# Optimization experiments

Measured on AMD Instinct MI355X. Metric: run time of the kernel, lower is better.

The kernel has to match this reference:

```python
import jax, jax.numpy as jnp
import numpy as np

BETA = 0.25
EPS_NORM = 1e-12   # matches torch F.normalize eps
EPS_COS = 1e-6     # clamp floor for cos weight


def _l2_normalize(v, axis=-1):
    n = jnp.linalg.norm(v, axis=axis, keepdims=True)
    return v / jnp.maximum(n, EPS_NORM)


def setup_inputs() -> dict:
    key = jax.random.key(0)
    kx, kc = jax.random.split(key)
    x = jax.random.normal(kx, (64, 1024, 256), dtype=jnp.float32)
    codebook = jax.random.normal(kc, (4096, 256), dtype=jnp.float32)
    return {"x": x, "codebook": codebook}


def reference(x, codebook):
    # Normalize codebook rows (F.normalize(codebook, dim=-1)).
    cb_n = _l2_normalize(codebook)                     # [K, D]
    # Cosine distance: 1 - cos_sim(x, cb). Only sim matters for argmin.
    x_n = _l2_normalize(x)                             # [B, S, D]
    sim = jnp.einsum('bsd,kd->bsk', x_n, cb_n)         # [B, S, K]
    dists = 1.0 - sim
    ids = jnp.argmin(dists, axis=-1)                   # [B, S] int
    c_k = cb_n[ids]                                    # [B, S, D] gather
    # Cosine weight uses RAW x (x_norm = x in the torch code).
    cos_k = jnp.sum(x * c_k, axis=-1, keepdims=True)   # [B, S, 1]
    cos_k = jnp.maximum(cos_k, EPS_COS)
    weighted_emb = cos_k * c_k                         # [B, S, D]
    # Cosine quantization loss: codebook term + beta * commitment term,
    # each 1 - cos_sim with stop-gradient on the opposite operand.
    def cos_sim(a, b):
        return jnp.sum(_l2_normalize(a) * _l2_normalize(b), axis=-1)
    codebook_term = jnp.mean(1.0 - cos_sim(jax.lax.stop_gradient(x), c_k))
    commit_term = jnp.mean(1.0 - cos_sim(x, jax.lax.stop_gradient(c_k)))
    loss = codebook_term + BETA * commit_term
    return ids, weighted_emb, loss
```

## Files before the change

kernel.cpp:

```cpp
#include <hip/hip_runtime.h>
#include <math.h>
#include <stdint.h>


#define TOKENS 65536
#define DIM 256
#define KCB 4096

#define TB 256
#define DELTA_SCALE 0.03125f
#define LIST_CAP (1u << 21)
#define SCAP 4096
#define RBLOCKS 2048

typedef short bf16x8 __attribute__((ext_vector_type(8)));
typedef float f32x4 __attribute__((ext_vector_type(4)));

__device__ inline short f2bf(float f) {
    uint32_t u = __float_as_uint(f);
    u += 0x7FFF + ((u >> 16) & 1);
    return (short)(u >> 16);
}

__global__ void prep_all(const float* __restrict__ cb, const float* __restrict__ x,
                         float* __restrict__ cbn, short* __restrict__ cbh2,
                         float* __restrict__ xnorm, float* __restrict__ invnx) {
    int bid  = blockIdx.x;
    int w    = threadIdx.x >> 6;
    int lane = threadIdx.x & 63;
    if (bid < KCB / 4) {
        int row = bid * 4 + w;
        float4 v = *(const float4*)(cb + (size_t)row * DIM + lane * 4);
        float ss = v.x * v.x + v.y * v.y + v.z * v.z + v.w * v.w;
#pragma unroll
        for (int off = 32; off; off >>= 1) ss += __shfl_xor(ss, off);
        float scale = 1.0f / fmaxf(sqrtf(ss), 1e-12f);
        float4 o = {v.x * scale, v.y * scale, v.z * scale, v.w * scale};
        *(float4*)(cbn + (size_t)row * DIM + lane * 4) = o;
        short4 h = {f2bf(o.x), f2bf(o.y), f2bf(o.z), f2bf(o.w)};
        int g = row >> 4, l15 = row & 15;
        int kst = lane >> 3, q = (lane >> 1) & 3, jhalf = lane & 1;
        size_t dst = ((size_t)((g * 8 + kst) * 64 + q * 16 + l15)) * 8 + jhalf * 4;
        *(short4*)(cbh2 + dst) = h;
    } else {
        int row = (bid - KCB / 4) * 4 + w;
        float4 v = *(const float4*)(x + (size_t)row * DIM + lane * 4);
        float ss = v.x * v.x + v.y * v.y + v.z * v.z + v.w * v.w;
#pragma unroll
        for (int off = 32; off; off >>= 1) ss += __shfl_xor(ss, off);
        if (lane == 0) {
            float n = fmaxf(sqrtf(ss), 1e-12f);
            xnorm[row] = n;
            invnx[row] = 1.0f / n;
        }
    }
}

#define LOADB(buf, cti)                                                            \
    {                                                                              \
        const short* bp_ = cbh2 + (size_t)(ch * 128 + (cti)) * 4096 + lane * 8;    \
        _Pragma("unroll")                                                          \
        for (int j = 0; j < 8; ++j) buf[j] = *(const bf16x8*)(bp_ + j * 512);      \
    }

#define COMPUTE(buf)                                                               \
    {                                                                              \
        _Pragma("unroll")                                                          \
        for (int mf = 0; mf < 4; ++mf) acc[mf] = (f32x4){0.f, 0.f, 0.f, 0.f};      \
        _Pragma("unroll")                                                          \
        for (int kst = 0; kst < 8; ++kst)                                          \
            _Pragma("unroll")                                                      \
            for (int mf = 0; mf < 4; ++mf)                                         \
                acc[mf] = __builtin_amdgcn_mfma_f32_16x16x32_bf16(                 \
                    areg[mf][kst], buf[kst], acc[mf], 0, 0, 0);                    \
    }

#define FOLDMAX()                                                                  \
    {                                                                              \
        _Pragma("unroll")                                                          \
        for (int mf = 0; mf < 4; ++mf)                                             \
            _Pragma("unroll")                                                      \
            for (int r = 0; r < 4; ++r)                                            \
                rmax[mf][r] = fmaxf(rmax[mf][r], acc[mf][r]);                      \
    }

#define EXTRACT(cti)                                                               \
    {                                                                              \
        _Pragma("unroll")                                                          \
        for (int mf = 0; mf < 4; ++mf)                                             \
            _Pragma("unroll")                                                      \
            for (int r = 0; r < 4; ++r) {                                          \
                if (acc[mf][r] >= thr[mf][r]) {                                    \
                    uint32_t t = twb + mf * 16 + q * 4 + r;                        \
                    uint32_t c = ch * 2048 + (cti) * 16 + l15;                     \
                    uint32_t e = (t << 12) | c;                                    \
                    uint32_t idx = atomicAdd(&s_cnt, 1u);                          \
                    if (idx < SCAP) s_list[idx] = e;                               \
                    else { uint32_t g2 = atomicAdd(cnt, 1u);                       \
                           if (g2 < LIST_CAP) list[g2] = e; }                      \
                }                                                                  \
            }                                                                      \
    }

__global__ __launch_bounds__(512, 2) void mfma_select(
    const float* __restrict__ x, const short* __restrict__ cbh2,
    const float* __restrict__ xnorm,
    uint32_t* __restrict__ list, uint32_t* __restrict__ cnt) {
    __shared__ uint32_t s_list[SCAP];
    __shared__ uint32_t s_cnt, s_base;
    __shared__ float maxbuf[2][TB];

    const int tid  = threadIdx.x;
    const int lane = tid & 63;
    const int wid  = tid >> 6;
    const int tq   = wid >> 1;
    const int ch   = wid & 1;
    const int l15  = lane & 15, q = lane >> 4;
    const int tb   = blockIdx.x * TB;
    const int twb  = tb + tq * 64;

    if (tid == 0) s_cnt = 0;

    bf16x8 areg[4][8];
#pragma unroll
    for (int mf = 0; mf < 4; ++mf) {
        const float* xr = x + (size_t)(twb + mf * 16 + l15) * DIM + q * 8;
#pragma unroll
        for (int kst = 0; kst < 8; ++kst) {
            float4 f0 = *(const float4*)(xr + kst * 32);
            float4 f1 = *(const float4*)(xr + kst * 32 + 4);
            bf16x8 h;
            h[0] = f2bf(f0.x); h[1] = f2bf(f0.y); h[2] = f2bf(f0.z); h[3] = f2bf(f0.w);
            h[4] = f2bf(f1.x); h[5] = f2bf(f1.y); h[6] = f2bf(f1.z); h[7] = f2bf(f1.w);
            areg[mf][kst] = h;
        }
    }

    float rmax[4][4];
#pragma unroll
    for (int mf = 0; mf < 4; ++mf)
#pragma unroll
        for (int r = 0; r < 4; ++r) rmax[mf][r] = -3.0e38f;

    {
        bf16x8 bA[8], bB[8];
        f32x4 acc[4];
        LOADB(bA, 0)
        for (int ct = 0; ct < 128; ct += 2) {
            LOADB(bB, ct + 1)
            __builtin_amdgcn_sched_barrier(0);
            COMPUTE(bA)
            FOLDMAX()
            int ctn = (ct + 2 < 128) ? ct + 2 : 127;
            LOADB(bA, ctn)
            __builtin_amdgcn_sched_barrier(0);
            COMPUTE(bB)
            FOLDMAX()
        }
    }

#pragma unroll
    for (int mf = 0; mf < 4; ++mf)
#pragma unroll
        for (int r = 0; r < 4; ++r) {
            float v = rmax[mf][r];
#pragma unroll
            for (int o = 1; o < 16; o <<= 1) v = fmaxf(v, __shfl_xor(v, o));
            rmax[mf][r] = v;
        }
    if (l15 == 0) {
#pragma unroll
        for (int mf = 0; mf < 4; ++mf)
#pragma unroll
            for (int r = 0; r < 4; ++r)
                maxbuf[ch][tq * 64 + mf * 16 + q * 4 + r] = rmax[mf][r];
    }
    __syncthreads();
    float thr[4][4];
#pragma unroll
    for (int mf = 0; mf < 4; ++mf)
#pragma unroll
        for (int r = 0; r < 4; ++r) {
            int tl = tq * 64 + mf * 16 + q * 4 + r;
            thr[mf][r] = fmaxf(maxbuf[0][tl], maxbuf[1][tl])
                       - DELTA_SCALE * xnorm[tb + tl];
        }

    {
        bf16x8 bA[8], bB[8];
        f32x4 acc[4];
        LOADB(bA, 0)
        for (int ct = 0; ct < 128; ct += 2) {
            LOADB(bB, ct + 1)
            __builtin_amdgcn_sched_barrier(0);
            COMPUTE(bA)
            EXTRACT(ct)
            int ctn = (ct + 2 < 128) ? ct + 2 : 127;
            LOADB(bA, ctn)
            __builtin_amdgcn_sched_barrier(0);
            COMPUTE(bB)
            EXTRACT(ct + 1)
        }
    }

    __syncthreads();
    if (tid == 0) {
        uint32_t m = s_cnt;
        if (m > SCAP) m = SCAP;
        s_base = atomicAdd(cnt, m);
        s_cnt = m;
    }
    __syncthreads();
    for (uint32_t i = tid; i < s_cnt; i += 512) {
        uint32_t idx = s_base + i;
        if (idx < LIST_CAP) list[idx] = s_list[i];
    }
}

__global__ void rescore(const float* __restrict__ x, const float* __restrict__ cbn,
                        const float* __restrict__ invnx,
                        const uint32_t* __restrict__ list, const uint32_t* __restrict__ cnt,
                        unsigned long long* __restrict__ win) {
    uint32_t n = *cnt;
    if (n > LIST_CAP) n = LIST_CAP;
    uint32_t swz = (blockIdx.x & 7) * (RBLOCKS / 8) + (blockIdx.x >> 3);
    uint32_t per = (n + RBLOCKS - 1) / RBLOCKS;
    uint32_t lo  = swz * per;
    uint32_t hi  = lo + per;
    if (hi > n) hi = n;
    for (uint32_t e = lo + threadIdx.x; e < hi; e += blockDim.x) {
        uint32_t v = list[e];
        uint32_t t = v >> 12, c = v & 4095;
        const float4* xp = (const float4*)(x + (size_t)t * DIM);
        const float4* cp = (const float4*)(cbn + (size_t)c * DIM);
        float acc = 0.0f;
#pragma unroll 8
        for (int k = 0; k < DIM / 4; ++k) {
            float4 xv = xp[k];
            float4 cv = cp[k];
            acc = fmaf(xv.x, cv.x, acc);
            acc = fmaf(xv.y, cv.y, acc);
            acc = fmaf(xv.z, cv.z, acc);
            acc = fmaf(xv.w, cv.w, acc);
        }
        float s = acc * invnx[t];
        float dist = 1.0f - s;
        uint32_t u = __float_as_uint(dist);
        u = (u & 0x80000000u) ? ~u : (u | 0x80000000u);
        unsigned long long key = ((unsigned long long)u << 32) | c;
        atomicMin(win + t, key);
    }
}

__global__ void epilogue_kernel(const float* __restrict__ x, const float* __restrict__ cbn,
                                const float* __restrict__ invnx,
                                const unsigned long long* __restrict__ win,
                                float* __restrict__ ids_f,
                                float* __restrict__ emb, float* __restrict__ partials) {
    int w    = threadIdx.x >> 6;
    int lane = threadIdx.x & 63;
    int t    = blockIdx.x * 4 + w;
    int id   = (int)(win[t] & 0xFFFFFFFFull);
    if ((unsigned)id > 4095u) id = 0;
    if (lane == 0) ids_f[t] = (float)id;

    float4 c4 = *(const float4*)(cbn + (size_t)id * DIM + lane * 4);
    float4 x4 = *(const float4*)(x + (size_t)t * DIM + lane * 4);
    float dxc = c4.x * x4.x + c4.y * x4.y + c4.z * x4.z + c4.w * x4.w;
    float ssc = c4.x * c4.x + c4.y * c4.y + c4.z * c4.z + c4.w * c4.w;
#pragma unroll
    for (int off = 32; off; off >>= 1) {
        dxc += __shfl_xor(dxc, off);
        ssc += __shfl_xor(ssc, off);
    }
    float cosk = fmaxf(dxc, 1e-6f);
    float4 o = {cosk * c4.x, cosk * c4.y, cosk * c4.z, cosk * c4.w};
    *(float4*)(emb + (size_t)t * DIM + lane * 4) = o;

    float invnc = 1.0f / fmaxf(sqrtf(ssc), 1e-12f);
    float term = 1.0f - dxc * invnx[t] * invnc;

    __shared__ float sterm[4];
    if (lane == 0) sterm[w] = term;
    __syncthreads();
    if (threadIdx.x == 0)
        partials[blockIdx.x] = sterm[0] + sterm[1] + sterm[2] + sterm[3];
}

__global__ void finalize_kernel(const float* __restrict__ partials, float* __restrict__ loss) {
    __shared__ float buf[256];
    float s = 0.0f;
    for (int i = threadIdx.x; i < TOKENS / 4; i += 256) s += partials[i];
    buf[threadIdx.x] = s;
    __syncthreads();
    for (int st = 128; st; st >>= 1) {
        if (threadIdx.x < st) buf[threadIdx.x] += buf[threadIdx.x + st];
        __syncthreads();
    }
    if (threadIdx.x == 0) loss[0] = buf[0] * (1.25f / (float)TOKENS);
}

extern "C" void kernel_launch(void* const* d_in, const int* in_sizes, int n_in,
                              void* d_out, int out_size, void* d_ws, size_t ws_size,
                              hipStream_t stream) {
    const float* x  = (const float*)d_in[0];
    const float* cb = (const float*)d_in[1];

    float* out   = (float*)d_out;
    float* ids_f = out;
    float* emb   = out + TOKENS;
    float* loss  = out + TOKENS + (size_t)TOKENS * DIM;

    float* ws = (float*)d_ws;
    float* cbn   = ws;
    short* cbh2  = (short*)(cbn + (size_t)KCB * DIM);
    float* xnorm = (float*)(cbh2 + (size_t)KCB * DIM);
    float* invnx = xnorm + TOKENS;
    unsigned long long* win = (unsigned long long*)(invnx + TOKENS);
    uint32_t* list = (uint32_t*)(win + TOKENS);
    uint32_t* cnt  = list + LIST_CAP;
    float* partials = (float*)(cnt + 16);

    hipMemsetAsync(cnt, 0, 64, stream);
    hipMemsetAsync(win, 0xFF, sizeof(unsigned long long) * TOKENS, stream);

    prep_all<<<KCB / 4 + TOKENS / 4, 256, 0, stream>>>(cb, x, cbn, cbh2, xnorm, invnx);
    mfma_select<<<TOKENS / TB, 512, 0, stream>>>(x, cbh2, xnorm, list, cnt);
    rescore<<<RBLOCKS, 256, 0, stream>>>(x, cbn, invnx, list, cnt, win);
    epilogue_kernel<<<TOKENS / 4, 256, 0, stream>>>(x, cbn, invnx, win, ids_f, emb, partials);
    finalize_kernel<<<1, 256, 0, stream>>>(partials, loss);
}
```

Baseline: 404.6 us.

## Fuse candidate extraction into first MFMA pass using running-max threshold

```diff
diff --git a/kernel.cpp b/kernel.cpp
--- a/kernel.cpp
+++ b/kernel.cpp
@@ -10,7 +10,8 @@
 #define TB 256
 #define DELTA_SCALE 0.03125f
 #define LIST_CAP (1u << 21)
-#define SCAP 4096
+#define SCAP 8192
+#define PRIME 16
 #define RBLOCKS 2048
 
 typedef short bf16x8 __attribute__((ext_vector_type(8)));
@@ -20,6 +21,30 @@
     uint32_t u = __float_as_uint(f);
     u += 0x7FFF + ((u >> 16) & 1);
     return (short)(u >> 16);
+}
+
+__device__ inline void rescore_one(const float* __restrict__ x, const float* __restrict__ cbn,
+                                   const float* __restrict__ invnx,
+                                   unsigned long long* __restrict__ win,
+                                   uint32_t t, uint32_t c) {
+    const float4* xp = (const float4*)(x + (size_t)t * DIM);
+    const float4* cp = (const float4*)(cbn + (size_t)c * DIM);
+    float acc = 0.0f;
+#pragma unroll 8
+    for (int k = 0; k < DIM / 4; ++k) {
+        float4 xv = xp[k];
+        float4 cv = cp[k];
+        acc = fmaf(xv.x, cv.x, acc);
+        acc = fmaf(xv.y, cv.y, acc);
+        acc = fmaf(xv.z, cv.z, acc);
+        acc = fmaf(xv.w, cv.w, acc);
+    }
+    float s = acc * invnx[t];
+    float dist = 1.0f - s;
+    uint32_t u = __float_as_uint(dist);
+    u = (u & 0x80000000u) ? ~u : (u | 0x80000000u);
+    unsigned long long key = ((unsigned long long)u << 32) | c;
+    atomicMin(win + t, key);
 }
 
 __global__ void prep_all(const float* __restrict__ cb, const float* __restrict__ x,
@@ -84,28 +109,41 @@
                 rmax[mf][r] = fmaxf(rmax[mf][r], acc[mf][r]);                      \
     }
 
-#define EXTRACT(cti)                                                               \
+#define REFRESH()                                                                  \
     {                                                                              \
         _Pragma("unroll")                                                          \
         for (int mf = 0; mf < 4; ++mf)                                             \
             _Pragma("unroll")                                                      \
             for (int r = 0; r < 4; ++r) {                                          \
-                if (acc[mf][r] >= thr[mf][r]) {                                    \
+                float v = rmax[mf][r];                                             \
+                _Pragma("unroll")                                                  \
+                for (int o = 1; o < 16; o <<= 1) v = fmaxf(v, __shfl_xor(v, o));   \
+                thrv[mf][r] = v - xnd[mf][r];                                      \
+            }                                                                      \
+    }
+
+#define EXTRACT_V(cti, THR)                                                        \
+    {                                                                              \
+        _Pragma("unroll")                                                          \
+        for (int mf = 0; mf < 4; ++mf)                                             \
+            _Pragma("unroll")                                                      \
+            for (int r = 0; r < 4; ++r) {                                          \
+                if (acc[mf][r] >= THR[mf][r]) {                                    \
                     uint32_t t = twb + mf * 16 + q * 4 + r;                        \
                     uint32_t c = ch * 2048 + (cti) * 16 + l15;                     \
-                    uint32_t e = (t << 12) | c;                                    \
                     uint32_t idx = atomicAdd(&s_cnt, 1u);                          \
-                    if (idx < SCAP) s_list[idx] = e;                               \
-                    else { uint32_t g2 = atomicAdd(cnt, 1u);                       \
-                           if (g2 < LIST_CAP) list[g2] = e; }                      \
+                    if (idx < SCAP) s_list[idx] = (t << 12) | c;                   \
+                    else rescore_one(x, cbn, invnx, win, t, c);                    \
                 }                                                                  \
             }                                                                      \
     }
 
 __global__ __launch_bounds__(512, 2) void mfma_select(
     const float* __restrict__ x, const short* __restrict__ cbh2,
-    const float* __restrict__ xnorm,
-    uint32_t* __restrict__ list, uint32_t* __restrict__ cnt) {
+    const float* __restrict__ xnorm, const float* __restrict__ cbn,
+    const float* __restrict__ invnx,
+    uint32_t* __restrict__ list, uint32_t* __restrict__ cnt,
+    unsigned long long* __restrict__ win) {
     __shared__ uint32_t s_list[SCAP];
     __shared__ uint32_t s_cnt, s_base;
     __shared__ float maxbuf[2][TB];
@@ -136,25 +174,37 @@
         }
     }
 
-    float rmax[4][4];
+    float xnd[4][4];
 #pragma unroll
     for (int mf = 0; mf < 4; ++mf)
 #pragma unroll
-        for (int r = 0; r < 4; ++r) rmax[mf][r] = -3.0e38f;
+        for (int r = 0; r < 4; ++r)
+            xnd[mf][r] = DELTA_SCALE * xnorm[twb + mf * 16 + q * 4 + r];
+
+    __syncthreads();
+
+    float rmax[4][4], thrv[4][4];
+#pragma unroll
+    for (int mf = 0; mf < 4; ++mf)
+#pragma unroll
+        for (int r = 0; r < 4; ++r) { rmax[mf][r] = -3.0e38f; thrv[mf][r] = 3.0e38f; }
 
     {
         bf16x8 bA[8], bB[8];
         f32x4 acc[4];
         LOADB(bA, 0)
         for (int ct = 0; ct < 128; ct += 2) {
+            if ((ct & 15) == 0 && ct) REFRESH()
             LOADB(bB, ct + 1)
             __builtin_amdgcn_sched_barrier(0);
             COMPUTE(bA)
+            if (ct >= PRIME) EXTRACT_V(ct, thrv)
             FOLDMAX()
             int ctn = (ct + 2 < 128) ? ct + 2 : 127;
             LOADB(bA, ctn)
             __builtin_amdgcn_sched_barrier(0);
             COMPUTE(bB)
+            if (ct + 1 >= PRIME) EXTRACT_V(ct + 1, thrv)
             FOLDMAX()
         }
     }
@@ -182,24 +232,17 @@
 #pragma unroll
         for (int r = 0; r < 4; ++r) {
             int tl = tq * 64 + mf * 16 + q * 4 + r;
-            thr[mf][r] = fmaxf(maxbuf[0][tl], maxbuf[1][tl])
-                       - DELTA_SCALE * xnorm[tb + tl];
+            thr[mf][r] = fmaxf(maxbuf[0][tl], maxbuf[1][tl]) - xnd[mf][r];
         }
 
     {
-        bf16x8 bA[8], bB[8];
+        bf16x8 bA[8];
         f32x4 acc[4];
-        LOADB(bA, 0)
-        for (int ct = 0; ct < 128; ct += 2) {
-            LOADB(bB, ct + 1)
+        for (int ct = 0; ct < PRIME; ++ct) {
+            LOADB(bA, ct)
             __builtin_amdgcn_sched_barrier(0);
             COMPUTE(bA)
-            EXTRACT(ct)
-            int ctn = (ct + 2 < 128) ? ct + 2 : 127;
-            LOADB(bA, ctn)
-            __builtin_amdgcn_sched_barrier(0);
-            COMPUTE(bB)
-            EXTRACT(ct + 1)
+            EXTRACT_V(ct, thr)
         }
     }
 
@@ -230,25 +273,7 @@
     if (hi > n) hi = n;
     for (uint32_t e = lo + threadIdx.x; e < hi; e += blockDim.x) {
         uint32_t v = list[e];
-        uint32_t t = v >> 12, c = v & 4095;
-        const float4* xp = (const float4*)(x + (size_t)t * DIM);
-        const float4* cp = (const float4*)(cbn + (size_t)c * DIM);
-        float acc = 0.0f;
-#pragma unroll 8
-        for (int k = 0; k < DIM / 4; ++k) {
-            float4 xv = xp[k];
-            float4 cv = cp[k];
-            acc = fmaf(xv.x, cv.x, acc);
-            acc = fmaf(xv.y, cv.y, acc);
-            acc = fmaf(xv.z, cv.z, acc);
-            acc = fmaf(xv.w, cv.w, acc);
-        }
-        float s = acc * invnx[t];
-        float dist = 1.0f - s;
-        uint32_t u = __float_as_uint(dist);
-        u = (u & 0x80000000u) ? ~u : (u | 0x80000000u);
-        unsigned long long key = ((unsigned long long)u << 32) | c;
-        atomicMin(win + t, key);
+        rescore_one(x, cbn, invnx, win, v >> 12, v & 4095);
     }
 }
 
@@ -325,7 +350,7 @@
     hipMemsetAsync(win, 0xFF, sizeof(unsigned long long) * TOKENS, stream);
 
     prep_all<<<KCB / 4 + TOKENS / 4, 256, 0, stream>>>(cb, x, cbn, cbh2, xnorm, invnx);
-    mfma_select<<<TOKENS / TB, 512, 0, stream>>>(x, cbh2, xnorm, list, cnt);
+    mfma_select<<<TOKENS / TB, 512, 0, stream>>>(x, cbh2, xnorm, cbn, invnx, list, cnt, win);
     rescore<<<RBLOCKS, 256, 0, stream>>>(x, cbn, invnx, list, cnt, win);
     epilogue_kernel<<<TOKENS / 4, 256, 0, stream>>>(x, cbn, invnx, win, ids_f, emb, partials);
     finalize_kernel<<<1, 256, 0, stream>>>(partials, loss);
```

Measured after the change: 1.036 ms. +156.0%, slower.
